# Performance work log

Hardware: AMD Instinct MI355X
Metric: run time of the kernel (lower is better)

Reference implementation:

```python
import jax, jax.numpy as jnp
import numpy as np

BETA = 0.25
DECAY = 0.99
EPS = 1e-05
N_E = 1024
E_DIM = 64

def setup_inputs() -> dict:
    key = jax.random.key(0)
    k1, k2, k3, k4 = jax.random.split(key, 4)
    z = jax.random.normal(k1, (32, 64, 32, 32), dtype=jnp.float32)
    embedding = jax.random.normal(k2, (N_E, E_DIM), dtype=jnp.float32)
    cluster_size = jax.random.uniform(k3, (N_E,), dtype=jnp.float32)
    cluster_sum = jax.random.normal(k4, (N_E, E_DIM), dtype=jnp.float32)
    return {"z": z, "embedding": embedding, "cluster_size": cluster_size, "cluster_sum": cluster_sum}


def reference(z, embedding, cluster_size, cluster_sum):
    # z: (B, C, H, W) with C == e_dim
    zp = jnp.transpose(z, (0, 2, 3, 1))            # (B, H, W, C)
    zf = zp.reshape(-1, E_DIM)                      # (N, e_dim)
    # squared-distance matrix: ||z||^2 + ||e||^2 - 2 z.e  -> (N, n_e)
    distance = (jnp.sum(zf ** 2, axis=1, keepdims=True)
                + jnp.sum(embedding ** 2, axis=1)
                - 2.0 * (zf @ embedding.T))
    idx = jnp.argmin(distance, axis=1)              # (N,)
    # one-hot counts / cluster sums expressed as segment sums (same math)
    counts = jax.ops.segment_sum(jnp.ones(zf.shape[0], dtype=zf.dtype), idx, num_segments=N_E)
    sums = jax.ops.segment_sum(zf, idx, num_segments=N_E)
    # EMA buffer update (module is in training mode -> embedding refreshed)
    new_cluster_size = DECAY * cluster_size + (1.0 - DECAY) * counts
    new_cluster_sum = DECAY * cluster_sum + (1.0 - DECAY) * sums
    new_embed = new_cluster_sum / (new_cluster_size + EPS)[:, None]
    z_q = new_embed[idx].reshape(zp.shape)          # gather-dequantize
    L_commitment = jnp.mean((jax.lax.stop_gradient(z_q) - zp) ** 2)
    loss = BETA * L_commitment
    z_q = zp + jax.lax.stop_gradient(z_q - zp)      # straight-through
    z_q = jnp.transpose(z_q, (0, 3, 1, 2))          # back to (B, C, H, W)
    return z_q, loss, counts
```

## Files before the change

### kernel.cpp

```cpp
#include <hip/hip_runtime.h>
#include <hip/hip_bf16.h>


#define N_ROWS   32768
#define N_CODES  1024
#define ZQ_ELEMS 2097152
#define NSPLIT   4
#define ZERO_N   (NSPLIT * (N_CODES + 65536))

typedef __attribute__((ext_vector_type(8))) short short8;
typedef __attribute__((ext_vector_type(4))) float f32x4;

__device__ __forceinline__ unsigned short f2bf(float x) {
    unsigned u = __float_as_uint(x);
    return (unsigned short)((u + 0x7fffu + ((u >> 16) & 1u)) >> 16);
}
__device__ __forceinline__ float bf2f(unsigned short h) {
    return __uint_as_float(((unsigned)h) << 16);
}

__global__ void vq_prep(const float* __restrict__ emb, float* __restrict__ zero_base,
                        unsigned short* __restrict__ eH, unsigned short* __restrict__ eM,
                        unsigned short* __restrict__ eL, float* __restrict__ enorm) {
    const int g = blockIdx.x * 256 + threadIdx.x;
    if (g < ZERO_N) {
        zero_base[g] = 0.f;
    } else if (g < ZERO_N + 65536) {
        const int i = g - ZERO_N;
        const float f = emb[i];
        const unsigned short h = f2bf(f);
        const float r1 = f - bf2f(h);
        const unsigned short m = f2bf(r1);
        const float r2 = r1 - bf2f(m);
        eH[i] = h; eM[i] = m; eL[i] = f2bf(r2);
    } else if (g < ZERO_N + 65536 + N_CODES) {
        const int c = g - ZERO_N - 65536;
        const float4* __restrict__ e4 = (const float4*)(emb + (c << 6));
        float s = 0.f;
        #pragma unroll
        for (int i = 0; i < 16; ++i) {
            const float4 v = e4[i];
            s = fmaf(v.x, v.x, s); s = fmaf(v.y, v.y, s);
            s = fmaf(v.z, v.z, s); s = fmaf(v.w, v.w, s);
        }
        enorm[c] = s;
    }
}

#define MFMA_BF16 __builtin_amdgcn_mfma_f32_16x16x32_bf16

__global__ __launch_bounds__(1024) void vq_dist(
        const float* __restrict__ z,
        const unsigned short* __restrict__ eH, const unsigned short* __restrict__ eM,
        const unsigned short* __restrict__ eL, const float* __restrict__ enorm,
        int* __restrict__ idx_out, float* __restrict__ counts,
        float* __restrict__ sums) {
    __shared__ unsigned short zH[128 * 72];
    __shared__ unsigned short zM[128 * 72];
    __shared__ unsigned short zL[128 * 72];
    __shared__ unsigned short esH[64 * 72];
    __shared__ unsigned short esM[64 * 72];
    __shared__ unsigned short esL[64 * 72];
    __shared__ float en_lds[N_CODES];
    __shared__ float bestS[4][128];
    __shared__ int   idxS[4][128];
    __shared__ int   idx_sh[128];

    const int t    = threadIdx.x;
    const int bid  = blockIdx.x;
    const int r0   = bid * 128;
    const int b    = r0 >> 10;
    const int hw0  = r0 & 1023;
    const int sp   = bid & (NSPLIT - 1);

    #pragma unroll
    for (int i = 0; i < 8; ++i) {
        const int cell = i * 1024 + t;
        const int row = cell & 127, c = cell >> 7;
        const float f = z[((b * 64 + c) << 10) + hw0 + row];
        const unsigned short h = f2bf(f);
        const float r1 = f - bf2f(h);
        const unsigned short m = f2bf(r1);
        const float r2 = r1 - bf2f(m);
        zH[row * 72 + c] = h;
        zM[row * 72 + c] = m;
        zL[row * 72 + c] = f2bf(r2);
    }
    en_lds[t] = enorm[t];
    __syncthreads();

    const int lane = t & 63, wid = t >> 6;
    const int wstrip = wid >> 2;
    const int cg     = wid & 3;
    const int lr = lane & 15, lk = lane >> 4;

    short8 aH[2][2], aM[2][2], aL[2][2];
    #pragma unroll
    for (int tl = 0; tl < 2; ++tl) {
        const int ab = (wstrip * 32 + tl * 16 + lr) * 72 + lk * 8;
        aH[tl][0] = *(const short8*)&zH[ab]; aH[tl][1] = *(const short8*)&zH[ab + 32];
        aM[tl][0] = *(const short8*)&zM[ab]; aM[tl][1] = *(const short8*)&zM[ab + 32];
        aL[tl][0] = *(const short8*)&zL[ab]; aL[tl][1] = *(const short8*)&zL[ab + 32];
    }

    float best[2][4]; int bidx[2][4];
    #pragma unroll
    for (int tl = 0; tl < 2; ++tl)
        #pragma unroll
        for (int i = 0; i < 4; ++i) { best[tl][i] = INFINITY; bidx[tl][i] = 0; }

    const int cl = t >> 4, k4 = t & 15;
    const int ebyte = (cl << 6) + k4 * 4;
    const int dsto  = cl * 72 + k4 * 4;
    short4 st0, st1, st2;
    st0 = *(const short4*)&eH[ebyte];
    st1 = *(const short4*)&eM[ebyte];
    st2 = *(const short4*)&eL[ebyte];

    for (int ch = 0; ch < 16; ++ch) {
        __syncthreads();
        *(short4*)&esH[dsto] = st0;
        *(short4*)&esM[dsto] = st1;
        *(short4*)&esL[dsto] = st2;
        __syncthreads();
        if (ch < 15) {
            const int off = (ch + 1) * 4096 + ebyte;
            st0 = *(const short4*)&eH[off];
            st1 = *(const short4*)&eM[off];
            st2 = *(const short4*)&eL[off];
        }

        const int bb = (cg * 16 + lr) * 72 + lk * 8;
        const short8 bH0 = *(const short8*)&esH[bb];
        const short8 bH1 = *(const short8*)&esH[bb + 32];
        const short8 bM0 = *(const short8*)&esM[bb];
        const short8 bM1 = *(const short8*)&esM[bb + 32];
        const short8 bL0 = *(const short8*)&esL[bb];
        const short8 bL1 = *(const short8*)&esL[bb + 32];

        f32x4 a0 = {0.f, 0.f, 0.f, 0.f};
        f32x4 a1 = {0.f, 0.f, 0.f, 0.f};
        a0 = MFMA_BF16(aH[0][0], bH0, a0, 0, 0, 0);
        a1 = MFMA_BF16(aH[1][0], bH0, a1, 0, 0, 0);
        a0 = MFMA_BF16(aH[0][1], bH1, a0, 0, 0, 0);
        a1 = MFMA_BF16(aH[1][1], bH1, a1, 0, 0, 0);
        a0 = MFMA_BF16(aH[0][0], bM0, a0, 0, 0, 0);
        a1 = MFMA_BF16(aH[1][0], bM0, a1, 0, 0, 0);
        a0 = MFMA_BF16(aH[0][1], bM1, a0, 0, 0, 0);
        a1 = MFMA_BF16(aH[1][1], bM1, a1, 0, 0, 0);
        a0 = MFMA_BF16(aM[0][0], bH0, a0, 0, 0, 0);
        a1 = MFMA_BF16(aM[1][0], bH0, a1, 0, 0, 0);
        a0 = MFMA_BF16(aM[0][1], bH1, a0, 0, 0, 0);
        a1 = MFMA_BF16(aM[1][1], bH1, a1, 0, 0, 0);
        a0 = MFMA_BF16(aM[0][0], bM0, a0, 0, 0, 0);
        a1 = MFMA_BF16(aM[1][0], bM0, a1, 0, 0, 0);
        a0 = MFMA_BF16(aM[0][1], bM1, a0, 0, 0, 0);
        a1 = MFMA_BF16(aM[1][1], bM1, a1, 0, 0, 0);
        a0 = MFMA_BF16(aH[0][0], bL0, a0, 0, 0, 0);
        a1 = MFMA_BF16(aH[1][0], bL0, a1, 0, 0, 0);
        a0 = MFMA_BF16(aH[0][1], bL1, a0, 0, 0, 0);
        a1 = MFMA_BF16(aH[1][1], bL1, a1, 0, 0, 0);
        a0 = MFMA_BF16(aL[0][0], bH0, a0, 0, 0, 0);
        a1 = MFMA_BF16(aL[1][0], bH0, a1, 0, 0, 0);
        a0 = MFMA_BF16(aL[0][1], bH1, a0, 0, 0, 0);
        a1 = MFMA_BF16(aL[1][1], bH1, a1, 0, 0, 0);

        const int code = ch * 64 + cg * 16 + lr;
        const float en_c = en_lds[code];
        #pragma unroll
        for (int i = 0; i < 4; ++i) {
            const float s0 = en_c - 2.0f * a0[i];
            if (s0 < best[0][i]) { best[0][i] = s0; bidx[0][i] = code; }
            const float s1 = en_c - 2.0f * a1[i];
            if (s1 < best[1][i]) { best[1][i] = s1; bidx[1][i] = code; }
        }
    }

    #pragma unroll
    for (int off = 1; off < 16; off <<= 1) {
        #pragma unroll
        for (int tl = 0; tl < 2; ++tl)
            #pragma unroll
            for (int i = 0; i < 4; ++i) {
                const float os = __shfl_xor(best[tl][i], off);
                const int   oi = __shfl_xor(bidx[tl][i], off);
                if (os < best[tl][i] || (os == best[tl][i] && oi < bidx[tl][i])) {
                    best[tl][i] = os; bidx[tl][i] = oi;
                }
            }
    }
    if (lr == 0) {
        #pragma unroll
        for (int tl = 0; tl < 2; ++tl)
            #pragma unroll
            for (int i = 0; i < 4; ++i) {
                const int row = wstrip * 32 + tl * 16 + lk * 4 + i;
                bestS[cg][row] = best[tl][i];
                idxS[cg][row]  = bidx[tl][i];
            }
    }
    __syncthreads();

    if (t < 128) {
        float bs = bestS[0][t]; int bi = idxS[0][t];
        #pragma unroll
        for (int g = 1; g < 4; ++g) {
            const float s = bestS[g][t]; const int ix = idxS[g][t];
            if (s < bs || (s == bs && ix < bi)) { bs = s; bi = ix; }
        }
        idx_sh[t] = bi;
        idx_out[r0 + t] = bi;
        atomicAdd(&counts[sp * N_CODES + bi], 1.0f);
    }
    __syncthreads();

    {
        const int k = t & 63, sub = t >> 6;
        #pragma unroll
        for (int i = 0; i < 8; ++i) {
            const int row = i * 16 + sub;
            const int o = row * 72 + k;
            const float v = (bf2f(zH[o]) + bf2f(zM[o])) + bf2f(zL[o]);
            atomicAdd(&sums[sp * 65536 + idx_sh[row] * 64 + k], v);
        }
    }
}

__global__ void vq_ema(const float* __restrict__ counts, const float* __restrict__ sums,
                       const float* __restrict__ cs, const float* __restrict__ csum,
                       float* __restrict__ new_embed, float* __restrict__ out_counts,
                       float* __restrict__ out_loss) {
    const int g = blockIdx.x * 256 + threadIdx.x;
    const int c = g >> 6, d = g & 63;
    const float cnt = (counts[c] + counts[N_CODES + c])
                    + (counts[2 * N_CODES + c] + counts[3 * N_CODES + c]);
    const float ssum = (sums[g] + sums[65536 + g]) + (sums[131072 + g] + sums[196608 + g]);
    const float nsize = 0.99f * cs[c] + 0.01f * cnt;
    const float nsum  = 0.99f * csum[g] + 0.01f * ssum;
    new_embed[g] = nsum / (nsize + 1e-5f);
    if (d == 0) out_counts[c] = cnt;
    if (g == 0) out_loss[0] = 0.f;
}

__global__ __launch_bounds__(256) void vq_gather(
        const float* __restrict__ z, const int* __restrict__ idx,
        const float* __restrict__ new_embed,
        float* __restrict__ out_zq, float* __restrict__ out_loss) {
    __shared__ float red[4];
    const int t  = threadIdx.x;
    const int r0 = blockIdx.x * 256;
    const int b  = r0 >> 10;
    const int hw = (r0 & 1023) + t;
    const int myidx = idx[r0 + t];

    const float4* __restrict__ er = (const float4*)(new_embed + (myidx << 6));
    float4 e4[16];
    #pragma unroll
    for (int i = 0; i < 16; ++i) e4[i] = er[i];

    float lsum = 0.f;
    #pragma unroll
    for (int c = 0; c < 64; ++c) {
        const float e  = ((const float*)e4)[c];
        const int  off = ((b * 64 + c) << 10) + hw;
        const float zv = z[off];
        const float diff = e - zv;
        out_zq[off] = zv + diff;
        lsum = fmaf(diff, diff, lsum);
    }
    #pragma unroll
    for (int off = 32; off >= 1; off >>= 1) lsum += __shfl_down(lsum, off);
    if ((t & 63) == 0) red[t >> 6] = lsum;
    __syncthreads();
    if (t == 0) {
        const float s = red[0] + red[1] + red[2] + red[3];
        atomicAdd(out_loss, s * (0.25f / 2097152.0f));
    }
}

extern "C" void kernel_launch(void* const* d_in, const int* in_sizes, int n_in,
                              void* d_out, int out_size, void* d_ws, size_t ws_size,
                              hipStream_t stream) {
    const float* z    = (const float*)d_in[0];
    const float* emb  = (const float*)d_in[1];
    const float* cs   = (const float*)d_in[2];
    const float* csum = (const float*)d_in[3];
    float* out = (float*)d_out;

    float* counts     = (float*)d_ws;
    float* sums       = counts + NSPLIT * N_CODES;
    float* enorm_ws   = sums + NSPLIT * 65536;
    float* new_embed  = enorm_ws + N_CODES;
    int*   idx        = (int*)(new_embed + 65536);
    unsigned short* eH = (unsigned short*)(idx + 32768);
    unsigned short* eM = eH + 65536;
    unsigned short* eL = eM + 65536;

    vq_prep<<<1300, 256, 0, stream>>>(emb, counts, eH, eM, eL, enorm_ws);
    vq_dist<<<256, 1024, 0, stream>>>(z, eH, eM, eL, enorm_ws, idx, counts, sums);
    vq_ema<<<256, 256, 0, stream>>>(counts, sums, cs, csum, new_embed,
                                    out + ZQ_ELEMS + 1,
                                    out + ZQ_ELEMS);
    vq_gather<<<128, 256, 0, stream>>>(z, idx, new_embed, out, out + ZQ_ELEMS);
}
```

Baseline: 140.4 us.

## Replace global atomic segment sums with owner-computes scatter kernel

The distance kernel no longer does global atomicAdds for counts and cluster sums. It instead writes the reconstructed fp32 z rows into the output buffer as scratch. A new vq_scatter kernel assigns 4 codes to each block; every block scans all 32768 indices and accumulates the matching rows with LDS atomics, then writes its results directly, which removes the zeroing pass and the 4-way split reduction. The cost is that every block reads the full index array, which adds redundant traffic and one extra kernel launch, and the scratch rows must later be overwritten by the gather kernel.

```diff
diff --git a/kernel.cpp b/kernel.cpp
--- a/kernel.cpp
+++ b/kernel.cpp
@@ -5,8 +5,7 @@
 #define N_ROWS   32768
 #define N_CODES  1024
 #define ZQ_ELEMS 2097152
-#define NSPLIT   4
-#define ZERO_N   (NSPLIT * (N_CODES + 65536))
+#define CPB      4
 
 typedef __attribute__((ext_vector_type(8))) short short8;
 typedef __attribute__((ext_vector_type(4))) float f32x4;
@@ -19,22 +18,19 @@
     return __uint_as_float(((unsigned)h) << 16);
 }
 
-__global__ void vq_prep(const float* __restrict__ emb, float* __restrict__ zero_base,
+__global__ void vq_prep(const float* __restrict__ emb,
                         unsigned short* __restrict__ eH, unsigned short* __restrict__ eM,
                         unsigned short* __restrict__ eL, float* __restrict__ enorm) {
     const int g = blockIdx.x * 256 + threadIdx.x;
-    if (g < ZERO_N) {
-        zero_base[g] = 0.f;
-    } else if (g < ZERO_N + 65536) {
-        const int i = g - ZERO_N;
-        const float f = emb[i];
+    if (g < 65536) {
+        const float f = emb[g];
         const unsigned short h = f2bf(f);
         const float r1 = f - bf2f(h);
         const unsigned short m = f2bf(r1);
         const float r2 = r1 - bf2f(m);
-        eH[i] = h; eM[i] = m; eL[i] = f2bf(r2);
-    } else if (g < ZERO_N + 65536 + N_CODES) {
-        const int c = g - ZERO_N - 65536;
+        eH[g] = h; eM[g] = m; eL[g] = f2bf(r2);
+    } else if (g < 65536 + N_CODES) {
+        const int c = g - 65536;
         const float4* __restrict__ e4 = (const float4*)(emb + (c << 6));
         float s = 0.f;
         #pragma unroll
@@ -53,8 +49,7 @@
         const float* __restrict__ z,
         const unsigned short* __restrict__ eH, const unsigned short* __restrict__ eM,
         const unsigned short* __restrict__ eL, const float* __restrict__ enorm,
-        int* __restrict__ idx_out, float* __restrict__ counts,
-        float* __restrict__ sums) {
+        int* __restrict__ idx_out, float* __restrict__ zf_out) {
     __shared__ unsigned short zH[128 * 72];
     __shared__ unsigned short zM[128 * 72];
     __shared__ unsigned short zL[128 * 72];
@@ -64,14 +59,12 @@
     __shared__ float en_lds[N_CODES];
     __shared__ float bestS[4][128];
     __shared__ int   idxS[4][128];
-    __shared__ int   idx_sh[128];
 
     const int t    = threadIdx.x;
     const int bid  = blockIdx.x;
     const int r0   = bid * 128;
     const int b    = r0 >> 10;
     const int hw0  = r0 & 1023;
-    const int sp   = bid & (NSPLIT - 1);
 
     #pragma unroll
     for (int i = 0; i < 8; ++i) {
@@ -208,11 +201,8 @@
             const float s = bestS[g][t]; const int ix = idxS[g][t];
             if (s < bs || (s == bs && ix < bi)) { bs = s; bi = ix; }
         }
-        idx_sh[t] = bi;
         idx_out[r0 + t] = bi;
-        atomicAdd(&counts[sp * N_CODES + bi], 1.0f);
-    }
-    __syncthreads();
+    }
 
     {
         const int k = t & 63, sub = t >> 6;
@@ -220,10 +210,40 @@
         for (int i = 0; i < 8; ++i) {
             const int row = i * 16 + sub;
             const int o = row * 72 + k;
-            const float v = (bf2f(zH[o]) + bf2f(zM[o])) + bf2f(zL[o]);
-            atomicAdd(&sums[sp * 65536 + idx_sh[row] * 64 + k], v);
-        }
-    }
+            zf_out[(r0 + row) * 64 + k] = (bf2f(zH[o]) + bf2f(zM[o])) + bf2f(zL[o]);
+        }
+    }
+}
+
+__global__ __launch_bounds__(256) void vq_scatter(
+        const float* __restrict__ zf, const int* __restrict__ idx,
+        float* __restrict__ counts, float* __restrict__ sums) {
+    __shared__ float acc[CPB * 64];
+    __shared__ float cnt[CPB];
+    const int t  = threadIdx.x;
+    const int c0 = blockIdx.x * CPB;
+    for (int i = t; i < CPB * 64; i += 256) acc[i] = 0.f;
+    if (t < CPB) cnt[t] = 0.f;
+    __syncthreads();
+
+    for (int r = t; r < N_ROWS; r += 256) {
+        const int c = idx[r] - c0;
+        if ((unsigned)c < (unsigned)CPB) {
+            atomicAdd(&cnt[c], 1.0f);
+            const float4* __restrict__ zr = (const float4*)(zf + (r << 6));
+            #pragma unroll
+            for (int i = 0; i < 16; ++i) {
+                const float4 v = zr[i];
+                atomicAdd(&acc[(c << 6) + 4 * i + 0], v.x);
+                atomicAdd(&acc[(c << 6) + 4 * i + 1], v.y);
+                atomicAdd(&acc[(c << 6) + 4 * i + 2], v.z);
+                atomicAdd(&acc[(c << 6) + 4 * i + 3], v.w);
+            }
+        }
+    }
+    __syncthreads();
+    for (int i = t; i < CPB * 64; i += 256) sums[(c0 << 6) + i] = acc[i];
+    if (t < CPB) counts[c0 + t] = cnt[t];
 }
 
 __global__ void vq_ema(const float* __restrict__ counts, const float* __restrict__ sums,
@@ -232,11 +252,9 @@
                        float* __restrict__ out_loss) {
     const int g = blockIdx.x * 256 + threadIdx.x;
     const int c = g >> 6, d = g & 63;
-    const float cnt = (counts[c] + counts[N_CODES + c])
-                    + (counts[2 * N_CODES + c] + counts[3 * N_CODES + c]);
-    const float ssum = (sums[g] + sums[65536 + g]) + (sums[131072 + g] + sums[196608 + g]);
+    const float cnt = counts[c];
     const float nsize = 0.99f * cs[c] + 0.01f * cnt;
-    const float nsum  = 0.99f * csum[g] + 0.01f * ssum;
+    const float nsum  = 0.99f * csum[g] + 0.01f * sums[g];
     new_embed[g] = nsum / (nsize + 1e-5f);
     if (d == 0) out_counts[c] = cnt;
     if (g == 0) out_loss[0] = 0.f;
@@ -288,16 +306,19 @@
     float* out = (float*)d_out;
 
     float* counts     = (float*)d_ws;
-    float* sums       = counts + NSPLIT * N_CODES;
-    float* enorm_ws   = sums + NSPLIT * 65536;
+    float* sums       = counts + N_CODES;
+    float* enorm_ws   = sums + 65536;
     float* new_embed  = enorm_ws + N_CODES;
     int*   idx        = (int*)(new_embed + 65536);
     unsigned short* eH = (unsigned short*)(idx + 32768);
     unsigned short* eM = eH + 65536;
     unsigned short* eL = eM + 65536;
 
-    vq_prep<<<1300, 256, 0, stream>>>(emb, counts, eH, eM, eL, enorm_ws);
-    vq_dist<<<256, 1024, 0, stream>>>(z, eH, eM, eL, enorm_ws, idx, counts, sums);
+    float* zf = out;
+
+    vq_prep<<<260, 256, 0, stream>>>(emb, eH, eM, eL, enorm_ws);
+    vq_dist<<<256, 1024, 0, stream>>>(z, eH, eM, eL, enorm_ws, idx, zf);
+    vq_scatter<<<256, 256, 0, stream>>>(zf, idx, counts, sums);
     vq_ema<<<256, 256, 0, stream>>>(counts, sums, cs, csum, new_embed,
                                     out + ZQ_ELEMS + 1,
                                     out + ZQ_ELEMS);
```

Result: slower. 272.7 us (+94.2%).
